# Optimization experiments

Measured on AMD Instinct MI355X. Metric: run time of the kernel, lower is better.

The kernel has to match this reference:

```python
import jax, jax.numpy as jnp
import numpy as np

N = 6144
M_VID = 1024
M_AUD = 128
APPERTURE = 20
EPS = 1e-6


def setup_inputs() -> dict:
    key = jax.random.key(0)
    ks = jax.random.split(key, 16)
    s = 0.02
    inp = {
        "x": jax.random.normal(ks[0], (1, N, M_VID), dtype=jnp.float32),
        "x_audio": jax.random.normal(ks[1], (1, N, M_AUD), dtype=jnp.float32),
        "seq_len": N,
        "audio_len": N,
        # video self-attention (torch Linear convention: W is [out, in])
        "Wk_v": jax.random.normal(ks[2], (M_VID, M_VID), dtype=jnp.float32) * s,
        "Wq_v": jax.random.normal(ks[3], (M_VID, M_VID), dtype=jnp.float32) * s,
        "Wv_v": jax.random.normal(ks[4], (M_VID, M_VID), dtype=jnp.float32) * s,
        "Wo_v": jax.random.normal(ks[5], (M_VID, M_VID), dtype=jnp.float32) * s,
        # audio self-attention
        "Wk_a": jax.random.normal(ks[6], (M_AUD, M_AUD), dtype=jnp.float32) * s,
        "Wq_a": jax.random.normal(ks[7], (M_AUD, M_AUD), dtype=jnp.float32) * s,
        "Wv_a": jax.random.normal(ks[8], (M_AUD, M_AUD), dtype=jnp.float32) * s,
        "Wo_a": jax.random.normal(ks[9], (M_AUD, M_AUD), dtype=jnp.float32) * s,
        # MLP head
        "ka_w": jax.random.normal(ks[10], (1024, M_VID + M_AUD), dtype=jnp.float32) * s,
        "ka_b": jnp.zeros((1024,), dtype=jnp.float32),
        "kd_w": jax.random.normal(ks[11], (1, 1024), dtype=jnp.float32) * s,
        "kd_b": jnp.zeros((1,), dtype=jnp.float32),
        # layer norms
        "ln_y_g": jnp.ones((M_VID,), dtype=jnp.float32),
        "ln_y_b": jnp.zeros((M_VID,), dtype=jnp.float32),
        "ln_ya_g": jnp.ones((M_AUD,), dtype=jnp.float32),
        "ln_ya_b": jnp.zeros((M_AUD,), dtype=jnp.float32),
        "ln_ka_g": jnp.ones((1024,), dtype=jnp.float32),
        "ln_ka_b": jnp.zeros((1024,), dtype=jnp.float32),
    }
    return inp


def _layer_norm(x, g, b):
    mu = jnp.mean(x, axis=-1, keepdims=True)
    var = jnp.mean((x - mu) ** 2, axis=-1, keepdims=True)
    return (x - mu) / jnp.sqrt(var + EPS) * g + b


def _self_attention(x, Wk, Wq, Wv, Wo):
    # x: [N, d]
    n = x.shape[0]
    K = x @ Wk.T
    Q = (x @ Wq.T) * 0.06
    V = x @ Wv.T
    logits = Q @ K.T  # [N, N]
    # keep only |i-j| < apperture (trimask masks |i-j| >= apperture)
    idx = jnp.arange(n)
    band = jnp.abs(idx[:, None] - idx[None, :]) < APPERTURE
    logits = jnp.where(band, logits, -jnp.inf)
    att = jax.nn.softmax(logits, axis=-1)  # [N, N]
    # torch: y = (V^T @ att)^T == att^T @ V  (note the transpose on att!)
    y = att.T @ V
    return y @ Wo.T, att


def reference(x, x_audio, seq_len, audio_len,
              Wk_v, Wq_v, Wv_v, Wo_v,
              Wk_a, Wq_a, Wv_a, Wo_a,
              ka_w, ka_b, kd_w, kd_b,
              ln_y_g, ln_y_b, ln_ya_g, ln_ya_b, ln_ka_g, ln_ka_b):
    m = x.shape[2]
    m_audio = x_audio.shape[2]
    xf = x.reshape(-1, m)            # [N, 1024]
    xa = x_audio.reshape(-1, m_audio)  # [N, 128]

    y, att_w = _self_attention(xf, Wk_v, Wq_v, Wv_v, Wo_v)
    y = _layer_norm(y + xf, ln_y_g, ln_y_b)

    ya, att_wa = _self_attention(xa, Wk_a, Wq_a, Wv_a, Wo_a)
    ya = _layer_norm(ya + xa, ln_ya_g, ln_ya_b)

    y_comb = jnp.concatenate((y, ya), axis=1)        # [N, 1152]
    att_comb = jnp.concatenate((att_w, att_wa), axis=1)  # [N, 2N]

    h = jax.nn.relu(y_comb @ ka_w.T + ka_b)
    h = _layer_norm(h, ln_ka_g, ln_ka_b)
    score = jax.nn.sigmoid(h @ kd_w.T + kd_b)  # [N, 1]
    score = score.reshape(1, -1)               # [1, N]
    return score, att_comb
```

## Files before the change

kernel.cpp:

```cpp
#include <hip/hip_runtime.h>
#include <stdint.h>

typedef unsigned short u16;
typedef unsigned int u32;
typedef __attribute__((ext_vector_type(8))) short bf16x8;
typedef __attribute__((ext_vector_type(4))) short s16x4;
typedef __attribute__((ext_vector_type(4))) float f32x4;
typedef __attribute__((ext_vector_type(2))) float f32x2;

#define DEV __device__ __forceinline__

DEV u16 f2bf(float f) {
  union { float f; unsigned u; } v; v.f = f;
  unsigned r = v.u + 0x7fffu + ((v.u >> 16) & 1u);
  return (u16)(r >> 16);
}
DEV float bf2f(u16 h) {
  union { u32 u; float f; } v; v.u = ((u32)h) << 16; return v.f;
}
DEV float lo16(u32 w) { union { u32 u; float f; } v; v.u = w << 16; return v.f; }
DEV float hi16(u32 w) { union { u32 u; float f; } v; v.u = w & 0xFFFF0000u; return v.f; }
DEV int imax(int a, int b) { return a > b ? a : b; }
DEV int imin(int a, int b) { return a < b ? a : b; }

DEV void g2lds16(const u16* g, u16* l) {
  __builtin_amdgcn_global_load_lds(
      (const __attribute__((address_space(1))) void*)g,
      (__attribute__((address_space(3))) void*)l, 16, 0, 0);
}

#define NSEG 9
struct CastTab {
  const float* src[NSEG];
  u16* dst[NSEG];
  int start[NSEG + 1];
};

__global__ __launch_bounds__(256) void vas_cast(CastTab t, int total4) {
  int idx = blockIdx.x * 256 + threadIdx.x;
  if (idx >= total4) return;
  int s = 0;
#pragma unroll
  for (int k = 1; k < NSEG; ++k)
    if (idx >= t.start[k]) s = k;
  int local = idx - t.start[s];
  f32x4 f = ((const f32x4*)t.src[s])[local];
  s16x4 o;
  o.x = (short)f2bf(f.x);
  o.y = (short)f2bf(f.y);
  o.z = (short)f2bf(f.z);
  o.w = (short)f2bf(f.w);
  ((s16x4*)t.dst[s])[local] = o;
}

__global__ __launch_bounds__(256) void vas_transpose(
    const float* __restrict__ Vv, u16* __restrict__ Tv,
    const float* __restrict__ Va, u16* __restrict__ Ta, int nvb) {
  __shared__ float t[32][33];
  int b = blockIdx.x;
  const float* src; u16* dst; int n;
  if (b < nvb) { src = Vv; dst = Tv; n = 1024; }
  else { b -= nvb; src = Va; dst = Ta; n = 128; }
  const int tpr = n >> 5;
  const int tr = (b / tpr) * 32, tc = (b % tpr) * 32;
  const int lx = threadIdx.x & 31, ly = threadIdx.x >> 5;
#pragma unroll
  for (int r = 0; r < 4; ++r)
    t[ly + r * 8][lx] = src[(size_t)(tr + ly + r * 8) * n + tc + lx];
  __syncthreads();
#pragma unroll
  for (int r = 0; r < 4; ++r)
    dst[(size_t)(tc + ly + r * 8) * n + tr + lx] = f2bf(t[lx][ly + r * 8]);
}

struct GemmP {
  const u16* A;
  const u16* W;
  void* C;
  const float* bias;
  int M, Nn, K, mode;
};

__global__ __launch_bounds__(256) void vas_gemm2(GemmP p0, GemmP p1, int split) {
  const int nwg = gridDim.x;
  const int b0 = blockIdx.x;
  const int qq = nwg >> 3, rr = nwg & 7, xcd = b0 & 7, li = b0 >> 3;
  const int bs = (xcd < rr ? xcd * (qq + 1) : rr * (qq + 1) + (xcd - rr) * qq) + li;

  const bool first = bs < split;
  GemmP p = first ? p0 : p1;
  const int bid = first ? bs : bs - split;

  __shared__ u16 As[2][128 * 32];
  __shared__ u16 Ws[2][128 * 32];
  const int tid = threadIdx.x;
  const int lane = tid & 63;
  const int wave = tid >> 6;

  const int Mb = p.M >> 7, Nb = p.Nn >> 7;
  const int GM = 8;
  int per = GM * Nb;
  int g = bid / per;
  int rem = bid - g * per;
  int gm = imin(GM, Mb - g * GM);
  int mblk = g * GM + rem % gm;
  int nblk = rem / gm;
  const int m0 = mblk * 128;
  const int n0 = nblk * 128;
  const int wm = (wave >> 1) * 64;
  const int wn = (wave & 1) * 64;

  const int smat = wave >> 1;
  const int skh = wave & 1;
  const u16* ssrc = smat ? p.W : p.A;
  const int sbase = smat ? n0 : m0;
  u16* sdstBase = (smat ? &Ws[skh][0] : &As[skh][0]) + lane * 8;
  const int srow = lane >> 2;
  const int scol = (lane & 3) * 8;

  f32x4 acc[4][4] = {};

  for (int k0 = 0; k0 < p.K; k0 += 64) {
#pragma unroll
    for (int u = 0; u < 8; ++u) {
      int r0 = u * 16;
      g2lds16(ssrc + (size_t)(sbase + r0 + srow) * p.K + (k0 + skh * 32 + scol),
              sdstBase + r0 * 32);
    }
    __syncthreads();
#pragma unroll
    for (int kk = 0; kk < 2; ++kk) {
      bf16x8 af[4], bfr[4];
#pragma unroll
      for (int t = 0; t < 4; ++t)
        af[t] = *(const bf16x8*)(&As[kk][0] + (wm + t * 16 + (lane & 15)) * 32 + (lane >> 4) * 8);
#pragma unroll
      for (int t = 0; t < 4; ++t)
        bfr[t] = *(const bf16x8*)(&Ws[kk][0] + (wn + t * 16 + (lane & 15)) * 32 + (lane >> 4) * 8);
#pragma unroll
      for (int mi = 0; mi < 4; ++mi)
#pragma unroll
        for (int ni = 0; ni < 4; ++ni)
          acc[mi][ni] = __builtin_amdgcn_mfma_f32_16x16x32_bf16(af[mi], bfr[ni], acc[mi][ni], 0, 0, 0);
    }
    __syncthreads();
  }

#pragma unroll
  for (int mi = 0; mi < 4; ++mi) {
#pragma unroll
    for (int ni = 0; ni < 4; ++ni) {
      int col = n0 + wn + ni * 16 + (lane & 15);
      float bv = p.bias ? p.bias[col] : 0.f;
#pragma unroll
      for (int r = 0; r < 4; ++r) {
        int row = m0 + wm + mi * 16 + (lane >> 4) * 4 + r;
        float vv = acc[mi][ni][r] + bv;
        size_t idx = (size_t)row * p.Nn + col;
        if (p.mode == 0) ((float*)p.C)[idx] = vv;
        else if (p.mode == 1) ((u16*)p.C)[idx] = f2bf(fmaxf(vv, 0.f));
        else ((u16*)p.C)[idx] = f2bf(vv);
      }
    }
  }
}

__global__ __launch_bounds__(256) void vas_battn(
    const u16* __restrict__ QKVv, const u16* __restrict__ QKVa,
    float* __restrict__ bandV, float* __restrict__ bandA,
    float* __restrict__ attBase, int N, float scale, int vb) {
  const int lane = threadIdx.x & 63;
  const int wave = threadIdx.x >> 6;
  const bool video = blockIdx.x < (u32)vb;
  const int i = (video ? blockIdx.x : blockIdx.x - vb) * 4 + wave;
  const int lo = imax(i - 19, 0);
  const int hi = imin(i + 19, N - 1);
  const int nj = hi - lo + 1;
  float logit = 0.f;
  __shared__ float a_sh[4][40];

  if (video) {
    float qf[16];
    const u16* qrow = QKVv + (size_t)i * 3072 + 1024;
#pragma unroll
    for (int c = 0; c < 2; ++c) {
      bf16x8 qv = *(const bf16x8*)(qrow + c * 512 + lane * 8);
      const u32* qw = (const u32*)&qv;
#pragma unroll
      for (int t = 0; t < 4; ++t) {
        qf[c * 8 + 2 * t] = lo16(qw[t]);
        qf[c * 8 + 2 * t + 1] = hi16(qw[t]);
      }
    }
#pragma unroll 2
    for (int s = 0; s < nj; ++s) {
      const u16* kr = QKVv + (size_t)(lo + s) * 3072;
      float p = 0.f;
#pragma unroll
      for (int c = 0; c < 2; ++c) {
        bf16x8 kv = *(const bf16x8*)(kr + c * 512 + lane * 8);
        const u32* kw = (const u32*)&kv;
#pragma unroll
        for (int t = 0; t < 4; ++t)
          p += lo16(kw[t]) * qf[c * 8 + 2 * t] + hi16(kw[t]) * qf[c * 8 + 2 * t + 1];
      }
#pragma unroll
      for (int off = 32; off; off >>= 1) p += __shfl_xor(p, off);
      if (lane == s) logit = p;
    }
  } else {
    u32 q = *(const u32*)(QKVa + (size_t)i * 384 + 128 + lane * 2);
    float q0 = lo16(q), q1 = hi16(q);
#pragma unroll 2
    for (int s = 0; s < nj; ++s) {
      u32 k = *(const u32*)(QKVa + (size_t)(lo + s) * 384 + lane * 2);
      float p = lo16(k) * q0 + hi16(k) * q1;
#pragma unroll
      for (int off = 32; off; off >>= 1) p += __shfl_xor(p, off);
      if (lane == s) logit = p;
    }
  }

  logit *= scale;
  float v = (lane < nj) ? logit : -3.4e38f;
  float mx = v;
#pragma unroll
  for (int off = 32; off; off >>= 1) mx = fmaxf(mx, __shfl_xor(mx, off));
  float e = (lane < nj) ? __expf(v - mx) : 0.f;
  float den = e;
#pragma unroll
  for (int off = 32; off; off >>= 1) den += __shfl_xor(den, off);
  float att = (lane < nj) ? e / den : 0.f;
  float* band = video ? bandV : bandA;
  if (lane < 40) {
    band[i * 40 + lane] = att;
    a_sh[wave][lane] = att;
  }

  f32x4* rowp = (f32x4*)(attBase + (size_t)i * 2 * N + (video ? 0 : N));
  const int nchunks = N / 4;
  const int cLo = lo >> 2, cHi = hi >> 2;
  for (int c = lane; c < nchunks; c += 64) {
    f32x4 o = {0.f, 0.f, 0.f, 0.f};
    if (c >= cLo && c <= cHi) {
      int col0 = c * 4;
#pragma unroll
      for (int e2 = 0; e2 < 4; ++e2) {
        int col = col0 + e2;
        if (col >= lo && col <= hi) o[e2] = a_sh[wave][col - lo];
      }
    }
    rowp[c] = o;
  }
}

#define JT 8
__global__ __launch_bounds__(256) void vas_apply_ln(
    const u16* __restrict__ QKVv, const u16* __restrict__ QKVa,
    const float* __restrict__ bandV, const float* __restrict__ bandA,
    const float* __restrict__ Xv, const float* __restrict__ Xa,
    const float* __restrict__ gv, const float* __restrict__ bv_,
    const float* __restrict__ ga, const float* __restrict__ ba,
    u16* __restrict__ out, int outStride, int N, int vb) {
  const int tid = threadIdx.x;
  __shared__ float a_sh[(JT + 38) * JT];
  __shared__ float red[2][JT][4];

  if (blockIdx.x < (u32)vb) {
    const int j0 = blockIdx.x * JT;
    const int base = j0 - 19;
    for (int idx = tid; idx < (JT + 38) * JT; idx += 256) {
      int s = idx / JT, jj = idx % JT;
      int i = base + s;
      int j = j0 + jj;
      float w = 0.f;
      if (i >= 0 && i < N) {
        int d = j - i;
        if (d > -20 && d < 20) w = bandV[i * 40 + (j - imax(i - 19, 0))];
      }
      a_sh[s * JT + jj] = w;
    }
    __syncthreads();

    f32x4 acc[JT] = {};
    const int sLo = imax(0, -base);
    const int sHi = imin(JT + 38, N - base);
    s16x4 nxt = *(const s16x4*)(QKVv + (size_t)(base + sLo) * 3072 + 2048 + tid * 4);
    for (int s = sLo; s < sHi; ++s) {
      s16x4 raw = nxt;
      if (s + 1 < sHi)
        nxt = *(const s16x4*)(QKVv + (size_t)(base + s + 1) * 3072 + 2048 + tid * 4);
      f32x4 vv;
      vv.x = bf2f((u16)raw.x);
      vv.y = bf2f((u16)raw.y);
      vv.z = bf2f((u16)raw.z);
      vv.w = bf2f((u16)raw.w);
#pragma unroll
      for (int jj = 0; jj < JT; ++jj) {
        float a = a_sh[s * JT + jj];
        acc[jj].x += a * vv.x;
        acc[jj].y += a * vv.y;
        acc[jj].z += a * vv.z;
        acc[jj].w += a * vv.w;
      }
    }

    const int lane = tid & 63, wave = tid >> 6;
#pragma unroll
    for (int jj = 0; jj < JT; ++jj) {
      f32x4 x4 = ((const f32x4*)(Xv + (size_t)(j0 + jj) * 1024))[tid];
      f32x4 v;
      v.x = acc[jj].x + x4.x;
      v.y = acc[jj].y + x4.y;
      v.z = acc[jj].z + x4.z;
      v.w = acc[jj].w + x4.w;
      acc[jj] = v;
      float s = v.x + v.y + v.z + v.w;
      float s2 = v.x * v.x + v.y * v.y + v.z * v.z + v.w * v.w;
#pragma unroll
      for (int off = 32; off; off >>= 1) {
        s += __shfl_xor(s, off);
        s2 += __shfl_xor(s2, off);
      }
      if (lane == 0) { red[0][jj][wave] = s; red[1][jj][wave] = s2; }
    }
    __syncthreads();
    f32x4 gg = ((const f32x4*)gv)[tid];
    f32x4 bb = ((const f32x4*)bv_)[tid];
#pragma unroll
    for (int jj = 0; jj < JT; ++jj) {
      float S = red[0][jj][0] + red[0][jj][1] + red[0][jj][2] + red[0][jj][3];
      float S2 = red[1][jj][0] + red[1][jj][1] + red[1][jj][2] + red[1][jj][3];
      float mu = S / 1024.f;
      float var = S2 / 1024.f - mu * mu;
      float inv = rsqrtf(var + 1e-6f);
      f32x4 v = acc[jj];
      s16x4 o;
      o.x = (short)f2bf((v.x - mu) * inv * gg.x + bb.x);
      o.y = (short)f2bf((v.y - mu) * inv * gg.y + bb.y);
      o.z = (short)f2bf((v.z - mu) * inv * gg.z + bb.z);
      o.w = (short)f2bf((v.w - mu) * inv * gg.w + bb.w);
      *(s16x4*)(out + (size_t)(j0 + jj) * outStride + tid * 4) = o;
    }
  } else {
    const int lane = tid & 63;
    const int wave = tid >> 6;
    const int j = (blockIdx.x - vb) * 4 + wave;
    const int lo = imax(j - 19, 0);
    const int hi = imin(j + 19, N - 1);
    const int ni = hi - lo + 1;
    float* aw = a_sh + wave * 40;
    if (lane < ni) {
      int i = lo + lane;
      aw[lane] = bandA[i * 40 + (j - imax(i - 19, 0))];
    }
    __syncthreads();
    f32x2 acc = {0.f, 0.f};
#pragma unroll 4
    for (int s = 0; s < ni; ++s) {
      float a = aw[s];
      u32 k = *(const u32*)(QKVa + (size_t)(lo + s) * 384 + 256 + lane * 2);
      acc.x += a * lo16(k);
      acc.y += a * hi16(k);
    }
    f32x2 x2 = *(const f32x2*)(Xa + (size_t)j * 128 + lane * 2);
    float vx = acc.x + x2.x;
    float vy = acc.y + x2.y;
    float s = vx + vy, s2 = vx * vx + vy * vy;
#pragma unroll
    for (int off = 32; off; off >>= 1) {
      s += __shfl_xor(s, off);
      s2 += __shfl_xor(s2, off);
    }
    float mu = s / 128.f;
    float var = s2 / 128.f - mu * mu;
    float inv = rsqrtf(var + 1e-6f);
    f32x2 g2 = *(const f32x2*)(ga + lane * 2);
    f32x2 b2 = *(const f32x2*)(ba + lane * 2);
    u32 o = (u32)f2bf((vx - mu) * inv * g2.x + b2.x) |
            ((u32)f2bf((vy - mu) * inv * g2.y + b2.y) << 16);
    *(u32*)(out + (size_t)j * outStride + 1024 + lane * 2) = o;
  }
}

__global__ __launch_bounds__(256) void vas_head(
    const u16* __restrict__ H, const float* __restrict__ g,
    const float* __restrict__ bb, const float* __restrict__ kw,
    const float* __restrict__ kb, float* __restrict__ score) {
  const int row = blockIdx.x;
  const int tid = threadIdx.x, lane = tid & 63, wave = tid >> 6;
  __shared__ float shA[4], shB[4];
  s16x4 raw = ((const s16x4*)(H + (size_t)row * 1024))[tid];
  f32x4 v;
  v.x = bf2f((u16)raw.x);
  v.y = bf2f((u16)raw.y);
  v.z = bf2f((u16)raw.z);
  v.w = bf2f((u16)raw.w);
  float s = v.x + v.y + v.z + v.w;
  float s2 = v.x * v.x + v.y * v.y + v.z * v.z + v.w * v.w;
#pragma unroll
  for (int off = 32; off; off >>= 1) {
    s += __shfl_xor(s, off);
    s2 += __shfl_xor(s2, off);
  }
  if (lane == 0) { shA[wave] = s; shB[wave] = s2; }
  __syncthreads();
  float S = shA[0] + shA[1] + shA[2] + shA[3];
  float S2 = shB[0] + shB[1] + shB[2] + shB[3];
  float mu = S / 1024.f;
  float var = S2 / 1024.f - mu * mu;
  float inv = rsqrtf(var + 1e-6f);
  f32x4 gg = ((const f32x4*)g)[tid];
  f32x4 bv = ((const f32x4*)bb)[tid];
  f32x4 kv = ((const f32x4*)kw)[tid];
  float p = ((v.x - mu) * inv * gg.x + bv.x) * kv.x +
            ((v.y - mu) * inv * gg.y + bv.y) * kv.y +
            ((v.z - mu) * inv * gg.z + bv.z) * kv.z +
            ((v.w - mu) * inv * gg.w + bv.w) * kv.w;
#pragma unroll
  for (int off = 32; off; off >>= 1) p += __shfl_xor(p, off);
  __syncthreads();
  if (lane == 0) shA[wave] = p;
  __syncthreads();
  if (tid == 0) {
    float P = shA[0] + shA[1] + shA[2] + shA[3] + kb[0];
    score[row] = 1.f / (1.f + __expf(-P));
  }
}

extern "C" void kernel_launch(void* const* d_in, const int* in_sizes, int n_in,
                              void* d_out, int out_size, void* d_ws, size_t ws_size,
                              hipStream_t stream) {
  const float* x = (const float*)d_in[0];
  const float* xa = (const float*)d_in[1];
  const float* Wk_v = (const float*)d_in[4];
  const float* Wq_v = (const float*)d_in[5];
  const float* Wv_v = (const float*)d_in[6];
  const float* Wo_v = (const float*)d_in[7];
  const float* Wk_a = (const float*)d_in[8];
  const float* Wq_a = (const float*)d_in[9];
  const float* Wv_a = (const float*)d_in[10];
  const float* Wo_a = (const float*)d_in[11];
  const float* ka_w = (const float*)d_in[12];
  const float* ka_b = (const float*)d_in[13];
  const float* kd_w = (const float*)d_in[14];
  const float* kd_b = (const float*)d_in[15];
  const float* ln_y_g = (const float*)d_in[16];
  const float* ln_y_b = (const float*)d_in[17];
  const float* ln_ya_g = (const float*)d_in[18];
  const float* ln_ya_b = (const float*)d_in[19];
  const float* ln_ka_g = (const float*)d_in[20];
  const float* ln_ka_b = (const float*)d_in[21];

  const int N = in_sizes[0] / 1024;
  const int MV = 1024, MA = 128, MH = 1152;

  char* wsb = (char*)d_ws;
  size_t off = 0;
  auto alloc = [&](size_t bytes) -> void* {
    void* p = wsb + off;
    off += (bytes + 255) & ~(size_t)255;
    return p;
  };
  u16* xf_b    = (u16*)alloc((size_t)N * MV * 2);
  u16* xa_b    = (u16*)alloc((size_t)N * MA * 2);
  u16* wqkv_b  = (u16*)alloc((size_t)3 * MV * MV * 2);
  u16* wqkva_b = (u16*)alloc((size_t)3 * MA * MA * 2);
  u16* wov_b   = (u16*)alloc((size_t)MV * MV * 2);
  u16* woa_b   = (u16*)alloc((size_t)MA * MA * 2);
  u16* wvT_b   = (u16*)alloc((size_t)MV * MV * 2);
  u16* wvaT_b  = (u16*)alloc((size_t)MA * MA * 2);
  u16* kaw_b   = (u16*)alloc((size_t)1024 * MH * 2);
  u16* QKVv    = (u16*)alloc((size_t)N * 3 * MV * 2);
  u16* QKVa    = (u16*)alloc((size_t)N * 3 * MA * 2);
  float* bandV = (float*)alloc((size_t)N * 40 * 4);
  float* bandA = (float*)alloc((size_t)N * 40 * 4);
  u16* ycomb_b = (u16*)alloc((size_t)N * MH * 2);
  u16* h_b = (u16*)alloc((size_t)N * 1024 * 2);

  float* dout = (float*)d_out;
  float* attBase = dout + N;

  {
    CastTab t;
    int c = 0, cum = 0;
    auto seg = [&](const float* s, u16* d, size_t n) {
      t.src[c] = s; t.dst[c] = d; t.start[c] = cum; cum += (int)(n / 4); ++c;
    };
    seg(x, xf_b, (size_t)N * MV);
    seg(xa, xa_b, (size_t)N * MA);
    seg(Wk_v, wqkv_b + 0 * MV * MV, (size_t)MV * MV);
    seg(Wq_v, wqkv_b + 1 * MV * MV, (size_t)MV * MV);
    seg(Wk_a, wqkva_b + 0 * MA * MA, (size_t)MA * MA);
    seg(Wq_a, wqkva_b + 1 * MA * MA, (size_t)MA * MA);
    seg(Wo_v, wov_b, (size_t)MV * MV);
    seg(Wo_a, woa_b, (size_t)MA * MA);
    seg(ka_w, kaw_b, (size_t)1024 * MH);
    t.start[c] = cum;
    vas_cast<<<(cum + 255) / 256, 256, 0, stream>>>(t, cum);
  }

  {
    int nvb = (MV / 32) * (MV / 32);
    int nab = (MA / 32) * (MA / 32);
    vas_transpose<<<nvb + nab, 256, 0, stream>>>(Wv_v, wvT_b, Wv_a, wvaT_b, nvb);
  }

  {
    GemmP pv = {wov_b, wvT_b, wqkv_b + 2 * MV * MV, nullptr, MV, MV, MV, 2};
    GemmP pa = {woa_b, wvaT_b, wqkva_b + 2 * MA * MA, nullptr, MA, MA, MA, 2};
    int bv = (MV / 128) * (MV / 128);
    vas_gemm2<<<bv + 1, 256, 0, stream>>>(pv, pa, bv);
  }

  {
    GemmP pv = {xf_b, wqkv_b, QKVv, nullptr, N, 3 * MV, MV, 2};
    GemmP pa = {xa_b, wqkva_b, QKVa, nullptr, N, 3 * MA, MA, 2};
    int bv = (N / 128) * (3 * MV / 128);
    int ba = (N / 128) * (3 * MA / 128);
    vas_gemm2<<<bv + ba, 256, 0, stream>>>(pv, pa, bv);
  }

  vas_battn<<<N / 2, 256, 0, stream>>>(QKVv, QKVa, bandV, bandA, attBase, N, 0.06f, N / 4);

  vas_apply_ln<<<N / JT + N / 4, 256, 0, stream>>>(
      QKVv, QKVa, bandV, bandA, x, xa,
      ln_y_g, ln_y_b, ln_ya_g, ln_ya_b, ycomb_b, MH, N, N / JT);

  {
    GemmP ph = {ycomb_b, kaw_b, h_b, ka_b, N, 1024, MH, 1};
    int bh = (N / 128) * (1024 / 128);
    vas_gemm2<<<bh, 256, 0, stream>>>(ph, ph, bh);
  }

  vas_head<<<N, 256, 0, stream>>>(h_b, ln_ka_g, ln_ka_b, kd_w, kd_b, dout);
}
```

Baseline: 588.8 us.

## Fold Wq and Wk into a combined matrix to drop Q projection

```diff
diff --git a/kernel.cpp b/kernel.cpp
--- a/kernel.cpp
+++ b/kernel.cpp
@@ -29,7 +29,7 @@
       (__attribute__((address_space(3))) void*)l, 16, 0, 0);
 }
 
-#define NSEG 9
+#define NSEG 5
 struct CastTab {
   const float* src[NSEG];
   u16* dst[NSEG];
@@ -53,14 +53,24 @@
   ((s16x4*)t.dst[s])[local] = o;
 }
 
-__global__ __launch_bounds__(256) void vas_transpose(
-    const float* __restrict__ Vv, u16* __restrict__ Tv,
-    const float* __restrict__ Va, u16* __restrict__ Ta, int nvb) {
+struct TransTab {
+  const float* src[6];
+  u16* dst[6];
+  int n[6];
+  int start[7];
+};
+
+__global__ __launch_bounds__(256) void vas_trans(TransTab tt) {
   __shared__ float t[32][33];
   int b = blockIdx.x;
-  const float* src; u16* dst; int n;
-  if (b < nvb) { src = Vv; dst = Tv; n = 1024; }
-  else { b -= nvb; src = Va; dst = Ta; n = 128; }
+  int s = 0;
+#pragma unroll
+  for (int k = 1; k < 6; ++k)
+    if (b >= tt.start[k]) s = k;
+  b -= tt.start[s];
+  const float* src = tt.src[s];
+  u16* dst = tt.dst[s];
+  const int n = tt.n[s];
   const int tpr = n >> 5;
   const int tr = (b / tpr) * 32, tc = (b % tpr) * 32;
   const int lx = threadIdx.x & 31, ly = threadIdx.x >> 5;
@@ -81,15 +91,19 @@
   int M, Nn, K, mode;
 };
 
-__global__ __launch_bounds__(256) void vas_gemm2(GemmP p0, GemmP p1, int split) {
+__global__ __launch_bounds__(256) void vas_gemm4(
+    GemmP p0, GemmP p1, GemmP p2, GemmP p3, int s1, int s2, int s3) {
   const int nwg = gridDim.x;
   const int b0 = blockIdx.x;
   const int qq = nwg >> 3, rr = nwg & 7, xcd = b0 & 7, li = b0 >> 3;
   const int bs = (xcd < rr ? xcd * (qq + 1) : rr * (qq + 1) + (xcd - rr) * qq) + li;
 
-  const bool first = bs < split;
-  GemmP p = first ? p0 : p1;
-  const int bid = first ? bs : bs - split;
+  GemmP p;
+  int bid;
+  if (bs < s1) { p = p0; bid = bs; }
+  else if (bs < s2) { p = p1; bid = bs - s1; }
+  else if (bs < s3) { p = p2; bid = bs - s2; }
+  else { p = p3; bid = bs - s3; }
 
   __shared__ u16 As[2][128 * 32];
   __shared__ u16 Ws[2][128 * 32];
@@ -166,7 +180,8 @@
 }
 
 __global__ __launch_bounds__(256) void vas_battn(
-    const u16* __restrict__ QKVv, const u16* __restrict__ QKVa,
+    const u16* __restrict__ Xv, const u16* __restrict__ Xa,
+    const u16* __restrict__ KKVv, const u16* __restrict__ KKVa,
     float* __restrict__ bandV, float* __restrict__ bandA,
     float* __restrict__ attBase, int N, float scale, int vb) {
   const int lane = threadIdx.x & 63;
@@ -181,7 +196,7 @@
 
   if (video) {
     float qf[16];
-    const u16* qrow = QKVv + (size_t)i * 3072 + 1024;
+    const u16* qrow = Xv + (size_t)i * 1024;
 #pragma unroll
     for (int c = 0; c < 2; ++c) {
       bf16x8 qv = *(const bf16x8*)(qrow + c * 512 + lane * 8);
@@ -194,7 +209,7 @@
     }
 #pragma unroll 2
     for (int s = 0; s < nj; ++s) {
-      const u16* kr = QKVv + (size_t)(lo + s) * 3072;
+      const u16* kr = KKVv + (size_t)(lo + s) * 2048;
       float p = 0.f;
 #pragma unroll
       for (int c = 0; c < 2; ++c) {
@@ -209,11 +224,11 @@
       if (lane == s) logit = p;
     }
   } else {
-    u32 q = *(const u32*)(QKVa + (size_t)i * 384 + 128 + lane * 2);
+    u32 q = *(const u32*)(Xa + (size_t)i * 128 + lane * 2);
     float q0 = lo16(q), q1 = hi16(q);
 #pragma unroll 2
     for (int s = 0; s < nj; ++s) {
-      u32 k = *(const u32*)(QKVa + (size_t)(lo + s) * 384 + lane * 2);
+      u32 k = *(const u32*)(KKVa + (size_t)(lo + s) * 256 + lane * 2);
       float p = lo16(k) * q0 + hi16(k) * q1;
 #pragma unroll
       for (int off = 32; off; off >>= 1) p += __shfl_xor(p, off);
@@ -256,7 +271,7 @@
 
 #define JT 8
 __global__ __launch_bounds__(256) void vas_apply_ln(
-    const u16* __restrict__ QKVv, const u16* __restrict__ QKVa,
+    const u16* __restrict__ KKVv, const u16* __restrict__ KKVa,
     const float* __restrict__ bandV, const float* __restrict__ bandA,
     const float* __restrict__ Xv, const float* __restrict__ Xa,
     const float* __restrict__ gv, const float* __restrict__ bv_,
@@ -285,11 +300,11 @@
     f32x4 acc[JT] = {};
     const int sLo = imax(0, -base);
     const int sHi = imin(JT + 38, N - base);
-    s16x4 nxt = *(const s16x4*)(QKVv + (size_t)(base + sLo) * 3072 + 2048 + tid * 4);
+    s16x4 nxt = *(const s16x4*)(KKVv + (size_t)(base + sLo) * 2048 + 1024 + tid * 4);
     for (int s = sLo; s < sHi; ++s) {
       s16x4 raw = nxt;
       if (s + 1 < sHi)
-        nxt = *(const s16x4*)(QKVv + (size_t)(base + s + 1) * 3072 + 2048 + tid * 4);
+        nxt = *(const s16x4*)(KKVv + (size_t)(base + s + 1) * 2048 + 1024 + tid * 4);
       f32x4 vv;
       vv.x = bf2f((u16)raw.x);
       vv.y = bf2f((u16)raw.y);
@@ -359,7 +374,7 @@
 #pragma unroll 4
     for (int s = 0; s < ni; ++s) {
       float a = aw[s];
-      u32 k = *(const u32*)(QKVa + (size_t)(lo + s) * 384 + 256 + lane * 2);
+      u32 k = *(const u32*)(KKVa + (size_t)(lo + s) * 256 + 128 + lane * 2);
       acc.x += a * lo16(k);
       acc.y += a * hi16(k);
     }
@@ -462,17 +477,21 @@
     off += (bytes + 255) & ~(size_t)255;
     return p;
   };
-  u16* xf_b    = (u16*)alloc((size_t)N * MV * 2);
-  u16* xa_b    = (u16*)alloc((size_t)N * MA * 2);
-  u16* wqkv_b  = (u16*)alloc((size_t)3 * MV * MV * 2);
-  u16* wqkva_b = (u16*)alloc((size_t)3 * MA * MA * 2);
-  u16* wov_b   = (u16*)alloc((size_t)MV * MV * 2);
-  u16* woa_b   = (u16*)alloc((size_t)MA * MA * 2);
-  u16* wvT_b   = (u16*)alloc((size_t)MV * MV * 2);
-  u16* wvaT_b  = (u16*)alloc((size_t)MA * MA * 2);
-  u16* kaw_b   = (u16*)alloc((size_t)1024 * MH * 2);
-  u16* QKVv    = (u16*)alloc((size_t)N * 3 * MV * 2);
-  u16* QKVa    = (u16*)alloc((size_t)N * 3 * MA * 2);
+  u16* xf_b   = (u16*)alloc((size_t)N * MV * 2);
+  u16* xa_b   = (u16*)alloc((size_t)N * MA * 2);
+  u16* wov_b  = (u16*)alloc((size_t)MV * MV * 2);
+  u16* woa_b  = (u16*)alloc((size_t)MA * MA * 2);
+  u16* wqTv   = (u16*)alloc((size_t)MV * MV * 2);
+  u16* wkTv   = (u16*)alloc((size_t)MV * MV * 2);
+  u16* wvTv   = (u16*)alloc((size_t)MV * MV * 2);
+  u16* wqTa   = (u16*)alloc((size_t)MA * MA * 2);
+  u16* wkTa   = (u16*)alloc((size_t)MA * MA * 2);
+  u16* wvTa   = (u16*)alloc((size_t)MA * MA * 2);
+  u16* wWv    = (u16*)alloc((size_t)2 * MV * MV * 2);
+  u16* wWa    = (u16*)alloc((size_t)2 * MA * MA * 2);
+  u16* kaw_b  = (u16*)alloc((size_t)1024 * MH * 2);
+  u16* KKVv   = (u16*)alloc((size_t)N * 2 * MV * 2);
+  u16* KKVa   = (u16*)alloc((size_t)N * 2 * MA * 2);
   float* bandV = (float*)alloc((size_t)N * 40 * 4);
   float* bandA = (float*)alloc((size_t)N * 40 * 4);
   u16* ycomb_b = (u16*)alloc((size_t)N * MH * 2);
@@ -489,10 +508,6 @@
     };
     seg(x, xf_b, (size_t)N * MV);
     seg(xa, xa_b, (size_t)N * MA);
-    seg(Wk_v, wqkv_b + 0 * MV * MV, (size_t)MV * MV);
-    seg(Wq_v, wqkv_b + 1 * MV * MV, (size_t)MV * MV);
-    seg(Wk_a, wqkva_b + 0 * MA * MA, (size_t)MA * MA);
-    seg(Wq_a, wqkva_b + 1 * MA * MA, (size_t)MA * MA);
     seg(Wo_v, wov_b, (size_t)MV * MV);
     seg(Wo_a, woa_b, (size_t)MA * MA);
     seg(ka_w, kaw_b, (size_t)1024 * MH);
@@ -501,36 +516,50 @@
   }
 
   {
-    int nvb = (MV / 32) * (MV / 32);
-    int nab = (MA / 32) * (MA / 32);
-    vas_transpose<<<nvb + nab, 256, 0, stream>>>(Wv_v, wvT_b, Wv_a, wvaT_b, nvb);
+    TransTab tt;
+    int c = 0, cum = 0;
+    auto seg = [&](const float* s, u16* d, int n) {
+      tt.src[c] = s; tt.dst[c] = d; tt.n[c] = n; tt.start[c] = cum;
+      cum += (n / 32) * (n / 32); ++c;
+    };
+    seg(Wq_v, wqTv, MV);
+    seg(Wk_v, wkTv, MV);
+    seg(Wv_v, wvTv, MV);
+    seg(Wq_a, wqTa, MA);
+    seg(Wk_a, wkTa, MA);
+    seg(Wv_a, wvTa, MA);
+    tt.start[c] = cum;
+    vas_trans<<<cum, 256, 0, stream>>>(tt);
   }
 
   {
-    GemmP pv = {wov_b, wvT_b, wqkv_b + 2 * MV * MV, nullptr, MV, MV, MV, 2};
-    GemmP pa = {woa_b, wvaT_b, wqkva_b + 2 * MA * MA, nullptr, MA, MA, MA, 2};
-    int bv = (MV / 128) * (MV / 128);
-    vas_gemm2<<<bv + 1, 256, 0, stream>>>(pv, pa, bv);
+    GemmP gv = {wqTv, wkTv, wWv, nullptr, MV, MV, MV, 2};
+    GemmP uv = {wov_b, wvTv, wWv + (size_t)MV * MV, nullptr, MV, MV, MV, 2};
+    GemmP ga = {wqTa, wkTa, wWa, nullptr, MA, MA, MA, 2};
+    GemmP ua = {woa_b, wvTa, wWa + (size_t)MA * MA, nullptr, MA, MA, MA, 2};
+    int bg = (MV / 128) * (MV / 128);
+    vas_gemm4<<<2 * bg + 2, 256, 0, stream>>>(gv, uv, ga, ua, bg, 2 * bg, 2 * bg + 1);
   }
 
   {
-    GemmP pv = {xf_b, wqkv_b, QKVv, nullptr, N, 3 * MV, MV, 2};
-    GemmP pa = {xa_b, wqkva_b, QKVa, nullptr, N, 3 * MA, MA, 2};
-    int bv = (N / 128) * (3 * MV / 128);
-    int ba = (N / 128) * (3 * MA / 128);
-    vas_gemm2<<<bv + ba, 256, 0, stream>>>(pv, pa, bv);
-  }
-
-  vas_battn<<<N / 2, 256, 0, stream>>>(QKVv, QKVa, bandV, bandA, attBase, N, 0.06f, N / 4);
+    GemmP pv = {xf_b, wWv, KKVv, nullptr, N, 2 * MV, MV, 2};
+    GemmP pa = {xa_b, wWa, KKVa, nullptr, N, 2 * MA, MA, 2};
+    int bv = (N / 128) * (2 * MV / 128);
+    int ba = (N / 128) * (2 * MA / 128);
+    vas_gemm4<<<bv + ba, 256, 0, stream>>>(pv, pa, pa, pa, bv, bv + ba, bv + ba);
+  }
+
+  vas_battn<<<N / 2, 256, 0, stream>>>(xf_b, xa_b, KKVv, KKVa, bandV, bandA,
+                                       attBase, N, 0.06f, N / 4);
 
   vas_apply_ln<<<N / JT + N / 4, 256, 0, stream>>>(
-      QKVv, QKVa, bandV, bandA, x, xa,
+      KKVv, KKVa, bandV, bandA, x, xa,
       ln_y_g, ln_y_b, ln_ya_g, ln_ya_b, ycomb_b, MH, N, N / JT);
 
   {
     GemmP ph = {ycomb_b, kaw_b, h_b, ka_b, N, 1024, MH, 1};
     int bh = (N / 128) * (1024 / 128);
-    vas_gemm2<<<bh, 256, 0, stream>>>(ph, ph, bh);
+    vas_gemm4<<<bh, 256, 0, stream>>>(ph, ph, ph, ph, bh, bh, bh);
   }
 
   vas_head<<<N, 256, 0, stream>>>(h_b, ln_ka_g, ln_ka_b, kd_w, kd_b, dout);
```

After: 579.8 us. Within noise of the previous version (-1.5%).
